# Kernel tuning notes

Measured on AMD Instinct MI355X. Metric: run time of the kernel, lower is better.

## Reference

```python
import jax, jax.numpy as jnp
import numpy as np

B, S, D = 2, 2048, 2048
H, KVH, HD = 32, 8, 64
ROPE_THETA = 500000.0


def _rope_cos_sin(seq_len, head_dim, theta, batch):
    inv_freq = 1.0 / (theta ** (jnp.arange(0, head_dim, 2, dtype=jnp.float32) / head_dim))  # [HD/2]
    pos = jnp.arange(seq_len, dtype=jnp.float32)
    freqs = jnp.outer(pos, inv_freq)                      # [S, HD/2]
    emb = jnp.concatenate([freqs, freqs], axis=-1)        # [S, HD]
    cos = jnp.broadcast_to(jnp.cos(emb), (batch, seq_len, head_dim))
    sin = jnp.broadcast_to(jnp.sin(emb), (batch, seq_len, head_dim))
    return cos, sin


def setup_inputs() -> dict:
    key = jax.random.key(0)
    kx, kq, kk, kv, ko = jax.random.split(key, 5)
    x = jax.random.normal(kx, (B, S, D), dtype=jnp.float32)
    cos, sin = _rope_cos_sin(S, HD, ROPE_THETA, B)
    scale = 0.02
    Wq = jax.random.normal(kq, (H * HD, D), dtype=jnp.float32) * scale
    Wk = jax.random.normal(kk, (KVH * HD, D), dtype=jnp.float32) * scale
    Wv = jax.random.normal(kv, (KVH * HD, D), dtype=jnp.float32) * scale
    Wo = jax.random.normal(ko, (D, H * HD), dtype=jnp.float32) * scale
    return {"x": x, "cos": cos, "sin": sin, "Wq": Wq, "Wk": Wk, "Wv": Wv, "Wo": Wo}


def rotate_half(t):
    t1, t2 = jnp.split(t, 2, axis=-1)
    return jnp.concatenate([-t2, t1], axis=-1)


def reference(x, cos, sin, Wq, Wk, Wv, Wo):
    b, s, d = x.shape
    scaling = HD ** -0.5
    groups = H // KVH
    # projections (torch Linear: y = x @ W.T)
    q = jnp.einsum('bsd,od->bso', x, Wq).reshape(b, s, H, HD).transpose(0, 2, 1, 3)    # [B,H,S,HD]
    k = jnp.einsum('bsd,od->bso', x, Wk).reshape(b, s, KVH, HD).transpose(0, 2, 1, 3)  # [B,KVH,S,HD]
    v = jnp.einsum('bsd,od->bso', x, Wv).reshape(b, s, KVH, HD).transpose(0, 2, 1, 3)
    # RoPE (cos/sin unsqueezed over head dim)
    c = cos[:, None, :, :]
    sn = sin[:, None, :, :]
    q = q * c + rotate_half(q) * sn
    k = k * c + rotate_half(k) * sn
    # GQA: repeat kv heads
    k = jnp.repeat(k, groups, axis=1)  # [B,H,S,HD]
    v = jnp.repeat(v, groups, axis=1)
    # causal eager SDPA
    scores = jnp.einsum('bhqd,bhkd->bhqk', q, k) * scaling
    causal = jnp.tril(jnp.ones((s, s), dtype=bool))
    scores = jnp.where(causal[None, None], scores, jnp.finfo(scores.dtype).min)
    attn_weights = jax.nn.softmax(scores, axis=-1)
    attn = jnp.einsum('bhqk,bhkd->bhqd', attn_weights, v)
    attn = attn.transpose(0, 2, 1, 3).reshape(b, s, H * HD)
    out = jnp.einsum('bso,do->bsd', attn, Wo)
    return out
```

## Files before the change

### kernel.cpp

```cpp
#include <hip/hip_runtime.h>
#include <hip/hip_bf16.h>

typedef __attribute__((ext_vector_type(8))) short bf16x8_t;
typedef __attribute__((ext_vector_type(4))) float f32x4;

#define S_LEN  2048
#define NB     2
#define NH     32
#define NKVH   8
#define HD     64
#define DMODEL 2048
#define SCALE  0.125f

__device__ __forceinline__ void gload16(const __hip_bfloat16* g, __hip_bfloat16* l) {
  __builtin_amdgcn_global_load_lds(
      (const __attribute__((address_space(1))) void*)g,
      (__attribute__((address_space(3))) void*)l, 16, 0, 0);
}

struct CvtSeg { const float* src; __hip_bfloat16* dst; int n4; };
struct CvtArgs { CvtSeg s[5]; };

__global__ __launch_bounds__(256) void cvt_all(CvtArgs a) {
  int i = blockIdx.x * blockDim.x + threadIdx.x;
#pragma unroll
  for (int k = 0; k < 5; ++k) {
    if (i < a.s[k].n4) {
      float4 v = ((const float4*)a.s[k].src)[i];
      __hip_bfloat16 o0 = __float2bfloat16(v.x), o1 = __float2bfloat16(v.y);
      __hip_bfloat16 o2 = __float2bfloat16(v.z), o3 = __float2bfloat16(v.w);
      ushort4 pk;
      pk.x = *(unsigned short*)&o0; pk.y = *(unsigned short*)&o1;
      pk.z = *(unsigned short*)&o2; pk.w = *(unsigned short*)&o3;
      ((ushort4*)a.s[k].dst)[i] = pk;
      return;
    }
    i -= a.s[k].n4;
  }
}

__global__ __launch_bounds__(256)
void gemm_qkv(const __hip_bfloat16* __restrict__ A,
              const __hip_bfloat16* __restrict__ Wq,
              const __hip_bfloat16* __restrict__ Wk,
              const __hip_bfloat16* __restrict__ Wv,
              __hip_bfloat16* __restrict__ Qo,
              __hip_bfloat16* __restrict__ Ko,
              __hip_bfloat16* __restrict__ Vto,
              const float* __restrict__ cosb,
              const float* __restrict__ sinb)
{
  __shared__ __align__(16) __hip_bfloat16 As[2][128][32];
  __shared__ __align__(16) __hip_bfloat16 Bs[2][128][32];
  const int K = DMODEL;

  const int tid  = threadIdx.x;
  const int lane = tid & 63;
  const int w    = tid >> 6;
  const int wr   = (w >> 1) * 64;
  const int wc   = (w & 1) * 64;
  const int brow = blockIdx.y * 128;
  const int fr   = lane & 15;
  const int fg   = lane >> 4;

  const int bc = blockIdx.x * 128;
  const __hip_bfloat16* Bt; int bcol; int path;
  if (bc < 2048)      { Bt = Wq; bcol = bc;        path = 0; }
  else if (bc < 2560) { Bt = Wk; bcol = bc - 2048; path = 1; }
  else                { Bt = Wv; bcol = bc - 2560; path = 2; }

  const f32x4 fz = {0.f, 0.f, 0.f, 0.f};
  f32x4 acc[4][4];
#pragma unroll
  for (int i = 0; i < 4; ++i)
#pragma unroll
    for (int j = 0; j < 4; ++j) acc[i][j] = fz;

  const int lrow = lane >> 2;
  const int lcol = (lane & 3) * 8;
  const __hip_bfloat16* Ag = A  + (size_t)(brow + w * 32 + lrow) * K + lcol;
  const __hip_bfloat16* Bg = Bt + (size_t)(bcol + w * 32 + lrow) * K + lcol;

  auto stage = [&](int buf, int kt) {
    gload16(Ag + kt,                    &As[buf][w * 32][0]);
    gload16(Ag + (size_t)16 * K + kt,   &As[buf][w * 32 + 16][0]);
    gload16(Bg + kt,                    &Bs[buf][w * 32][0]);
    gload16(Bg + (size_t)16 * K + kt,   &Bs[buf][w * 32 + 16][0]);
  };

  stage(0, 0);
  __syncthreads();
  int cur = 0;
  for (int kt = 0; kt < K; kt += 32) {
    if (kt + 32 < K) stage(cur ^ 1, kt + 32);

    bf16x8_t af[4], bfr[4];
#pragma unroll
    for (int mi = 0; mi < 4; ++mi)
      af[mi] = *(const bf16x8_t*)&As[cur][wr + mi * 16 + fr][fg * 8];
#pragma unroll
    for (int ni = 0; ni < 4; ++ni)
      bfr[ni] = *(const bf16x8_t*)&Bs[cur][wc + ni * 16 + fr][fg * 8];
#pragma unroll
    for (int mi = 0; mi < 4; ++mi)
#pragma unroll
      for (int ni = 0; ni < 4; ++ni)
        acc[mi][ni] = __builtin_amdgcn_mfma_f32_16x16x32_bf16(af[mi], bfr[ni], acc[mi][ni], 0, 0, 0);

    __syncthreads();
    cur ^= 1;
  }

  if (path == 2) {
#pragma unroll
    for (int mi = 0; mi < 4; ++mi) {
#pragma unroll
      for (int ni = 0; ni < 4; ++ni) {
        const int row0 = brow + wr + mi * 16 + fg * 4;
        const int col  = bcol + wc + ni * 16 + fr;
        const int b = row0 >> 11, s = row0 & 2047;
        const int kvh = col >> 6, d = col & 63;
        __hip_bfloat16 v0 = __float2bfloat16(acc[mi][ni][0]);
        __hip_bfloat16 v1 = __float2bfloat16(acc[mi][ni][1]);
        __hip_bfloat16 v2 = __float2bfloat16(acc[mi][ni][2]);
        __hip_bfloat16 v3 = __float2bfloat16(acc[mi][ni][3]);
        ushort4 pk;
        pk.x = *(unsigned short*)&v0; pk.y = *(unsigned short*)&v1;
        pk.z = *(unsigned short*)&v2; pk.w = *(unsigned short*)&v3;
        *(ushort4*)&Vto[(((size_t)b * NKVH + kvh) * HD + d) * S_LEN + s] = pk;
      }
    }
  } else {
    __hip_bfloat16* C = (path == 0) ? Qo : Ko;
    const int N = (path == 0) ? (NH * HD) : (NKVH * HD);
#pragma unroll
    for (int mi = 0; mi < 4; ++mi) {
#pragma unroll
      for (int r = 0; r < 4; ++r) {
        const int row = brow + wr + mi * 16 + fg * 4 + r;
#pragma unroll
        for (int ni = 0; ni < 2; ++ni) {
          const int colL = bcol + wc + ni * 16 + fr;
          const int d    = (colL & 63);
          const float c  = cosb[(size_t)row * HD + d];
          const float sn = sinb[(size_t)row * HD + d];
          const float v0 = acc[mi][ni][r];
          const float v1 = acc[mi][ni + 2][r];
          C[(size_t)row * N + colL]      = __float2bfloat16(v0 * c - v1 * sn);
          C[(size_t)row * N + colL + 32] = __float2bfloat16(v1 * c + v0 * sn);
        }
      }
    }
  }
}

__global__ __launch_bounds__(256)
void gemm_o(const __hip_bfloat16* __restrict__ A,
            const __hip_bfloat16* __restrict__ Bt,
            float* __restrict__ C)
{
  __shared__ __align__(16) __hip_bfloat16 As[2][128][32];
  __shared__ __align__(16) __hip_bfloat16 Bs[2][128][32];
  const int K = DMODEL, N = DMODEL;

  const int tid  = threadIdx.x;
  const int lane = tid & 63;
  const int w    = tid >> 6;
  const int wr   = (w >> 1) * 64;
  const int wc   = (w & 1) * 64;
  const int brow = blockIdx.y * 128;
  const int bcol = blockIdx.x * 128;
  const int fr   = lane & 15;
  const int fg   = lane >> 4;

  const f32x4 fz = {0.f, 0.f, 0.f, 0.f};
  f32x4 acc[4][4];
#pragma unroll
  for (int i = 0; i < 4; ++i)
#pragma unroll
    for (int j = 0; j < 4; ++j) acc[i][j] = fz;

  const int lrow = lane >> 2;
  const int lcol = (lane & 3) * 8;
  const __hip_bfloat16* Ag = A  + (size_t)(brow + w * 32 + lrow) * K + lcol;
  const __hip_bfloat16* Bg = Bt + (size_t)(bcol + w * 32 + lrow) * K + lcol;

  auto stage = [&](int buf, int kt) {
    gload16(Ag + kt,                  &As[buf][w * 32][0]);
    gload16(Ag + (size_t)16 * K + kt, &As[buf][w * 32 + 16][0]);
    gload16(Bg + kt,                  &Bs[buf][w * 32][0]);
    gload16(Bg + (size_t)16 * K + kt, &Bs[buf][w * 32 + 16][0]);
  };

  stage(0, 0);
  __syncthreads();
  int cur = 0;
  for (int kt = 0; kt < K; kt += 32) {
    if (kt + 32 < K) stage(cur ^ 1, kt + 32);

    bf16x8_t af[4], bfr[4];
#pragma unroll
    for (int mi = 0; mi < 4; ++mi)
      af[mi] = *(const bf16x8_t*)&As[cur][wr + mi * 16 + fr][fg * 8];
#pragma unroll
    for (int ni = 0; ni < 4; ++ni)
      bfr[ni] = *(const bf16x8_t*)&Bs[cur][wc + ni * 16 + fr][fg * 8];
#pragma unroll
    for (int mi = 0; mi < 4; ++mi)
#pragma unroll
      for (int ni = 0; ni < 4; ++ni)
        acc[mi][ni] = __builtin_amdgcn_mfma_f32_16x16x32_bf16(af[mi], bfr[ni], acc[mi][ni], 0, 0, 0);

    __syncthreads();
    cur ^= 1;
  }

#pragma unroll
  for (int mi = 0; mi < 4; ++mi)
#pragma unroll
    for (int ni = 0; ni < 4; ++ni) {
      const int row0 = brow + wr + mi * 16 + fg * 4;
      const int col  = bcol + wc + ni * 16 + fr;
#pragma unroll
      for (int r = 0; r < 4; ++r)
        C[(size_t)(row0 + r) * N + col] = acc[mi][ni][r];
    }
}

__global__ __launch_bounds__(256)
void attn_kernel(const __hip_bfloat16* __restrict__ Q, const __hip_bfloat16* __restrict__ K,
                 const __hip_bfloat16* __restrict__ Vt, __hip_bfloat16* __restrict__ O)
{
  __shared__ __align__(16) __hip_bfloat16 Ks[2][64][64];
  __shared__ __align__(16) __hip_bfloat16 Vs[2][64][64];
  __shared__ __align__(16) __hip_bfloat16 Ps[4][2][16][72];

  const int lane = threadIdx.x & 63;
  const int w    = threadIdx.x >> 6;
  const int fr   = lane & 15;
  const int fg   = lane >> 4;
  const int r8   = lane >> 3;
  const int j8   = lane & 7;
  const int bh   = blockIdx.y;
  const int b    = bh >> 5;
  const int h    = bh & 31;
  const int kvh  = h >> 2;
  const int qt    = gridDim.x - 1 - blockIdx.x;
  const int qbase = qt * 128;

  const __hip_bfloat16* Qg = Q + ((size_t)(b * S_LEN + qbase)) * DMODEL + h * HD;
  const __hip_bfloat16* Kg = K + (size_t)b * S_LEN * (NKVH * HD) + kvh * HD;
  const __hip_bfloat16* Vg = Vt + ((size_t)(b * NKVH + kvh)) * HD * S_LEN;

  bf16x8_t qf[2][2];
#pragma unroll
  for (int s = 0; s < 2; ++s)
#pragma unroll
    for (int kk = 0; kk < 2; ++kk)
      qf[s][kk] = *(const bf16x8_t*)(Qg + (size_t)(w * 32 + s * 16 + fr) * DMODEL + kk * 32 + fg * 8);

  const f32x4 fz = {0.f, 0.f, 0.f, 0.f};
  f32x4 acc[2][4];
#pragma unroll
  for (int s = 0; s < 2; ++s)
#pragma unroll
    for (int i = 0; i < 4; ++i) acc[s][i] = fz;
  float m_[2] = {-1e30f, -1e30f}, l_[2] = {0.f, 0.f};

  auto stage = [&](int buf, int kt) {
#pragma unroll
    for (int half = 0; half < 2; ++half) {
      const int row = w * 16 + half * 8 + r8;
      gload16(Kg + (size_t)(kt + row) * (NKVH * HD) + (j8 ^ r8) * 8, &Ks[buf][w * 16 + half * 8][0]);
      gload16(Vg + (size_t)row * S_LEN + kt + (j8 ^ r8) * 8,         &Vs[buf][w * 16 + half * 8][0]);
    }
  };
  auto ldK = [&](int buf, int row, int cidx) -> bf16x8_t {
    return *(const bf16x8_t*)&Ks[buf][row][(cidx ^ (row & 7)) * 8];
  };
  auto ldV = [&](int buf, int row, int cidx) -> bf16x8_t {
    return *(const bf16x8_t*)&Vs[buf][row][(cidx ^ (row & 7)) * 8];
  };

  stage(0, 0);
  __syncthreads();
  int cur = 0;
  const int NT = 2 * qt + 2;
  for (int t = 0; t < NT; ++t) {
    const int kt = t * 64;
    if (t + 1 < NT) stage(cur ^ 1, kt + 64);

    f32x4 sc[2][4];
#pragma unroll
    for (int c = 0; c < 4; ++c) {
      const int krow = c * 16 + fr;
      bf16x8_t k0 = ldK(cur, krow, fg);
      bf16x8_t k1 = ldK(cur, krow, 4 + fg);
      sc[0][c] = __builtin_amdgcn_mfma_f32_16x16x32_bf16(k0, qf[0][0], fz, 0, 0, 0);
      sc[0][c] = __builtin_amdgcn_mfma_f32_16x16x32_bf16(k1, qf[0][1], sc[0][c], 0, 0, 0);
      sc[1][c] = __builtin_amdgcn_mfma_f32_16x16x32_bf16(k0, qf[1][0], fz, 0, 0, 0);
      sc[1][c] = __builtin_amdgcn_mfma_f32_16x16x32_bf16(k1, qf[1][1], sc[1][c], 0, 0, 0);
    }

#pragma unroll
    for (int s = 0; s < 2; ++s) {
      const int base_s = qbase + w * 32 + s * 16;
      float p[4][4];
      float tm = -1e30f;
      if (kt + 63 > base_s) {
#pragma unroll
        for (int c = 0; c < 4; ++c)
#pragma unroll
          for (int r = 0; r < 4; ++r) {
            float v = sc[s][c][r] * SCALE;
            if (kt + c * 16 + fg * 4 + r > base_s + fr) v = -1e30f;
            p[c][r] = v; tm = fmaxf(tm, v);
          }
      } else {
#pragma unroll
        for (int c = 0; c < 4; ++c)
#pragma unroll
          for (int r = 0; r < 4; ++r) {
            float v = sc[s][c][r] * SCALE;
            p[c][r] = v; tm = fmaxf(tm, v);
          }
      }
      tm = fmaxf(tm, __shfl_xor(tm, 16));
      tm = fmaxf(tm, __shfl_xor(tm, 32));

      const float mnew = fmaxf(m_[s], tm);
      const float sf = __expf(m_[s] - mnew);
      m_[s] = mnew;

      float ts = 0.f;
#pragma unroll
      for (int c = 0; c < 4; ++c)
#pragma unroll
        for (int r = 0; r < 4; ++r) { p[c][r] = __expf(p[c][r] - mnew); ts += p[c][r]; }
      ts += __shfl_xor(ts, 16);
      ts += __shfl_xor(ts, 32);
      l_[s] = l_[s] * sf + ts;

      float sfv[4];
#pragma unroll
      for (int r = 0; r < 4; ++r) sfv[r] = __shfl(sf, fg * 4 + r);
#pragma unroll
      for (int fc = 0; fc < 4; ++fc)
#pragma unroll
        for (int r = 0; r < 4; ++r) acc[s][fc][r] *= sfv[r];

#pragma unroll
      for (int c = 0; c < 4; ++c) {
        __hip_bfloat16 b0 = __float2bfloat16(p[c][0]);
        __hip_bfloat16 b1 = __float2bfloat16(p[c][1]);
        __hip_bfloat16 b2 = __float2bfloat16(p[c][2]);
        __hip_bfloat16 b3 = __float2bfloat16(p[c][3]);
        ushort4 pk;
        pk.x = *(unsigned short*)&b0; pk.y = *(unsigned short*)&b1;
        pk.z = *(unsigned short*)&b2; pk.w = *(unsigned short*)&b3;
        *(ushort4*)&Ps[w][s][fr][c * 16 + fg * 4] = pk;
      }
    }

#pragma unroll
    for (int kk = 0; kk < 2; ++kk) {
      bf16x8_t pa0 = *(const bf16x8_t*)&Ps[w][0][fr][kk * 32 + fg * 8];
      bf16x8_t pa1 = *(const bf16x8_t*)&Ps[w][1][fr][kk * 32 + fg * 8];
#pragma unroll
      for (int fc = 0; fc < 4; ++fc) {
        bf16x8_t vf = ldV(cur, fc * 16 + fr, kk * 4 + fg);
        acc[0][fc] = __builtin_amdgcn_mfma_f32_16x16x32_bf16(pa0, vf, acc[0][fc], 0, 0, 0);
        acc[1][fc] = __builtin_amdgcn_mfma_f32_16x16x32_bf16(pa1, vf, acc[1][fc], 0, 0, 0);
      }
    }

    __syncthreads();
    cur ^= 1;
  }

  float lv[2][4];
#pragma unroll
  for (int s = 0; s < 2; ++s)
#pragma unroll
    for (int r = 0; r < 4; ++r)
      lv[s][r] = __builtin_amdgcn_rcpf(__shfl(l_[s], fg * 4 + r));
#pragma unroll
  for (int s = 0; s < 2; ++s)
#pragma unroll
    for (int fc = 0; fc < 4; ++fc)
#pragma unroll
      for (int r = 0; r < 4; ++r) {
        const size_t row = (size_t)(b * S_LEN + qbase + w * 32 + s * 16 + fg * 4 + r);
        O[row * DMODEL + h * HD + fc * 16 + fr] = __float2bfloat16(acc[s][fc][r] * lv[s][r]);
      }
}

extern "C" void kernel_launch(void* const* d_in, const int* in_sizes, int n_in,
                              void* d_out, int out_size, void* d_ws, size_t ws_size,
                              hipStream_t stream)
{
  const float* x    = (const float*)d_in[0];
  const float* cosb = (const float*)d_in[1];
  const float* sinb = (const float*)d_in[2];
  const float* Wq   = (const float*)d_in[3];
  const float* Wk   = (const float*)d_in[4];
  const float* Wv   = (const float*)d_in[5];
  const float* Wo   = (const float*)d_in[6];
  float* out = (float*)d_out;

  char* p = (char*)d_ws;
  __hip_bfloat16* x_bf    = (__hip_bfloat16*)p; p += (size_t)NB * S_LEN * DMODEL * 2;
  __hip_bfloat16* Wq_bf   = (__hip_bfloat16*)p; p += (size_t)NH * HD * DMODEL * 2;
  __hip_bfloat16* Wk_bf   = (__hip_bfloat16*)p; p += (size_t)NKVH * HD * DMODEL * 2;
  __hip_bfloat16* Wv_bf   = (__hip_bfloat16*)p; p += (size_t)NKVH * HD * DMODEL * 2;
  __hip_bfloat16* Wo_bf   = (__hip_bfloat16*)p; p += (size_t)DMODEL * NH * HD * 2;
  __hip_bfloat16* Q_bf    = (__hip_bfloat16*)p; p += (size_t)NB * S_LEN * NH * HD * 2;
  __hip_bfloat16* K_bf    = (__hip_bfloat16*)p; p += (size_t)NB * S_LEN * NKVH * HD * 2;
  __hip_bfloat16* Vt_bf   = (__hip_bfloat16*)p; p += (size_t)NB * NKVH * HD * S_LEN * 2;
  __hip_bfloat16* attn_bf = (__hip_bfloat16*)p; p += (size_t)NB * S_LEN * NH * HD * 2;

  CvtArgs ca;
  ca.s[0] = { x,  x_bf,  (int)((size_t)NB * S_LEN * DMODEL / 4) };
  ca.s[1] = { Wq, Wq_bf, (int)((size_t)NH * HD * DMODEL / 4) };
  ca.s[2] = { Wk, Wk_bf, (int)((size_t)NKVH * HD * DMODEL / 4) };
  ca.s[3] = { Wv, Wv_bf, (int)((size_t)NKVH * HD * DMODEL / 4) };
  ca.s[4] = { Wo, Wo_bf, (int)((size_t)DMODEL * NH * HD / 4) };
  int total4 = ca.s[0].n4 + ca.s[1].n4 + ca.s[2].n4 + ca.s[3].n4 + ca.s[4].n4;
  cvt_all<<<(total4 + 255) / 256, 256, 0, stream>>>(ca);

  const dim3 blk(256);
  gemm_qkv<<<dim3(3072 / 128, (NB * S_LEN) / 128), blk, 0, stream>>>(
      x_bf, Wq_bf, Wk_bf, Wv_bf, Q_bf, K_bf, Vt_bf, cosb, sinb);

  attn_kernel<<<dim3(S_LEN / 128, NB * NH), blk, 0, stream>>>(Q_bf, K_bf, Vt_bf, attn_bf);

  gemm_o<<<dim3(DMODEL / 128, (NB * S_LEN) / 128), blk, 0, stream>>>(attn_bf, Wo_bf, out);
}
```

Before: 410.9 us.

## Use 8 waves per attention block with lazy rescale and exp2 softmax

The attention kernel now runs 512 threads per block, each wave owning 16 query rows instead of 32. K and V staging is split between the two halves of the block. Waves skip tiles that lie fully above the causal diagonal, and the running max is rescaled only when the new max exceeds the old one by a threshold. Exponentials use exp2 with the softmax scale folded into one constant, and the row-sum reduction across lanes is deferred to the end. This aims to raise occupancy, remove wasted masked work and cut per-tile rescale cost, at the price of per-wave divergence around barriers and the numerical risk of the lazy-rescale threshold.

```diff
diff --git a/kernel.cpp b/kernel.cpp
--- a/kernel.cpp
+++ b/kernel.cpp
@@ -11,6 +11,8 @@
 #define HD     64
 #define DMODEL 2048
 #define SCALE  0.125f
+#define CEXP   0.18033688f
+#define THRRAW 44.0f
 
 __device__ __forceinline__ void gload16(const __hip_bfloat16* g, __hip_bfloat16* l) {
   __builtin_amdgcn_global_load_lds(
@@ -227,13 +229,13 @@
     }
 }
 
-__global__ __launch_bounds__(256)
+__global__ __launch_bounds__(512, 6)
 void attn_kernel(const __hip_bfloat16* __restrict__ Q, const __hip_bfloat16* __restrict__ K,
                  const __hip_bfloat16* __restrict__ Vt, __hip_bfloat16* __restrict__ O)
 {
   __shared__ __align__(16) __hip_bfloat16 Ks[2][64][64];
   __shared__ __align__(16) __hip_bfloat16 Vs[2][64][64];
-  __shared__ __align__(16) __hip_bfloat16 Ps[4][2][16][72];
+  __shared__ __align__(16) __hip_bfloat16 Ps[8][16][72];
 
   const int lane = threadIdx.x & 63;
   const int w    = threadIdx.x >> 6;
@@ -247,32 +249,32 @@
   const int kvh  = h >> 2;
   const int qt    = gridDim.x - 1 - blockIdx.x;
   const int qbase = qt * 128;
+  const int base_s = qbase + w * 16;
 
   const __hip_bfloat16* Qg = Q + ((size_t)(b * S_LEN + qbase)) * DMODEL + h * HD;
   const __hip_bfloat16* Kg = K + (size_t)b * S_LEN * (NKVH * HD) + kvh * HD;
   const __hip_bfloat16* Vg = Vt + ((size_t)(b * NKVH + kvh)) * HD * S_LEN;
 
-  bf16x8_t qf[2][2];
-#pragma unroll
-  for (int s = 0; s < 2; ++s)
-#pragma unroll
-    for (int kk = 0; kk < 2; ++kk)
-      qf[s][kk] = *(const bf16x8_t*)(Qg + (size_t)(w * 32 + s * 16 + fr) * DMODEL + kk * 32 + fg * 8);
+  bf16x8_t qf[2];
+#pragma unroll
+  for (int kk = 0; kk < 2; ++kk)
+    qf[kk] = *(const bf16x8_t*)(Qg + (size_t)(w * 16 + fr) * DMODEL + kk * 32 + fg * 8);
 
   const f32x4 fz = {0.f, 0.f, 0.f, 0.f};
-  f32x4 acc[2][4];
-#pragma unroll
-  for (int s = 0; s < 2; ++s)
-#pragma unroll
-    for (int i = 0; i < 4; ++i) acc[s][i] = fz;
-  float m_[2] = {-1e30f, -1e30f}, l_[2] = {0.f, 0.f};
+  f32x4 acc[4];
+#pragma unroll
+  for (int i = 0; i < 4; ++i) acc[i] = fz;
+  float m_ = -1e30f;
+  float l_ = 0.f;
 
   auto stage = [&](int buf, int kt) {
-#pragma unroll
-    for (int half = 0; half < 2; ++half) {
-      const int row = w * 16 + half * 8 + r8;
-      gload16(Kg + (size_t)(kt + row) * (NKVH * HD) + (j8 ^ r8) * 8, &Ks[buf][w * 16 + half * 8][0]);
-      gload16(Vg + (size_t)row * S_LEN + kt + (j8 ^ r8) * 8,         &Vs[buf][w * 16 + half * 8][0]);
+    const int rb = (w & 3) * 16;
+    if (w < 4) {
+      gload16(Kg + (size_t)(kt + rb + r8)     * (NKVH * HD) + (j8 ^ r8) * 8, &Ks[buf][rb][0]);
+      gload16(Kg + (size_t)(kt + rb + 8 + r8) * (NKVH * HD) + (j8 ^ r8) * 8, &Ks[buf][rb + 8][0]);
+    } else {
+      gload16(Vg + (size_t)(rb + r8)     * S_LEN + kt + (j8 ^ r8) * 8, &Vs[buf][rb][0]);
+      gload16(Vg + (size_t)(rb + 8 + r8) * S_LEN + kt + (j8 ^ r8) * 8, &Vs[buf][rb + 8][0]);
     }
   };
   auto ldK = [&](int buf, int row, int cidx) -> bf16x8_t {
@@ -290,64 +292,60 @@
     const int kt = t * 64;
     if (t + 1 < NT) stage(cur ^ 1, kt + 64);
 
-    f32x4 sc[2][4];
-#pragma unroll
-    for (int c = 0; c < 4; ++c) {
-      const int krow = c * 16 + fr;
-      bf16x8_t k0 = ldK(cur, krow, fg);
-      bf16x8_t k1 = ldK(cur, krow, 4 + fg);
-      sc[0][c] = __builtin_amdgcn_mfma_f32_16x16x32_bf16(k0, qf[0][0], fz, 0, 0, 0);
-      sc[0][c] = __builtin_amdgcn_mfma_f32_16x16x32_bf16(k1, qf[0][1], sc[0][c], 0, 0, 0);
-      sc[1][c] = __builtin_amdgcn_mfma_f32_16x16x32_bf16(k0, qf[1][0], fz, 0, 0, 0);
-      sc[1][c] = __builtin_amdgcn_mfma_f32_16x16x32_bf16(k1, qf[1][1], sc[1][c], 0, 0, 0);
-    }
-
-#pragma unroll
-    for (int s = 0; s < 2; ++s) {
-      const int base_s = qbase + w * 32 + s * 16;
+    if (kt <= base_s + 15) {
+      f32x4 sc[4];
+#pragma unroll
+      for (int c = 0; c < 4; ++c) {
+        const int krow = c * 16 + fr;
+        bf16x8_t k0 = ldK(cur, krow, fg);
+        bf16x8_t k1 = ldK(cur, krow, 4 + fg);
+        sc[c] = __builtin_amdgcn_mfma_f32_16x16x32_bf16(k0, qf[0], fz, 0, 0, 0);
+        sc[c] = __builtin_amdgcn_mfma_f32_16x16x32_bf16(k1, qf[1], sc[c], 0, 0, 0);
+      }
+
       float p[4][4];
-      float tm = -1e30f;
+      float tm = -3.0e38f;
       if (kt + 63 > base_s) {
 #pragma unroll
         for (int c = 0; c < 4; ++c)
 #pragma unroll
           for (int r = 0; r < 4; ++r) {
-            float v = sc[s][c][r] * SCALE;
-            if (kt + c * 16 + fg * 4 + r > base_s + fr) v = -1e30f;
+            float v = sc[c][r];
+            if (kt + c * 16 + fg * 4 + r > base_s + fr) v = -3.0e38f;
             p[c][r] = v; tm = fmaxf(tm, v);
           }
       } else {
 #pragma unroll
         for (int c = 0; c < 4; ++c)
 #pragma unroll
-          for (int r = 0; r < 4; ++r) {
-            float v = sc[s][c][r] * SCALE;
-            p[c][r] = v; tm = fmaxf(tm, v);
-          }
+          for (int r = 0; r < 4; ++r) { p[c][r] = sc[c][r]; tm = fmaxf(tm, sc[c][r]); }
       }
       tm = fmaxf(tm, __shfl_xor(tm, 16));
       tm = fmaxf(tm, __shfl_xor(tm, 32));
 
-      const float mnew = fmaxf(m_[s], tm);
-      const float sf = __expf(m_[s] - mnew);
-      m_[s] = mnew;
+      if (!__all(tm <= m_ + THRRAW)) {
+        const float mnew = fmaxf(m_, tm);
+        const float sf = exp2f((m_ - mnew) * CEXP);
+        m_ = mnew;
+        l_ *= sf;
+        float sfv[4];
+#pragma unroll
+        for (int r = 0; r < 4; ++r) sfv[r] = __shfl(sf, fg * 4 + r);
+#pragma unroll
+        for (int fc = 0; fc < 4; ++fc)
+#pragma unroll
+          for (int r = 0; r < 4; ++r) acc[fc][r] *= sfv[r];
+      }
 
       float ts = 0.f;
 #pragma unroll
       for (int c = 0; c < 4; ++c)
 #pragma unroll
-        for (int r = 0; r < 4; ++r) { p[c][r] = __expf(p[c][r] - mnew); ts += p[c][r]; }
-      ts += __shfl_xor(ts, 16);
-      ts += __shfl_xor(ts, 32);
-      l_[s] = l_[s] * sf + ts;
-
-      float sfv[4];
-#pragma unroll
-      for (int r = 0; r < 4; ++r) sfv[r] = __shfl(sf, fg * 4 + r);
-#pragma unroll
-      for (int fc = 0; fc < 4; ++fc)
-#pragma unroll
-        for (int r = 0; r < 4; ++r) acc[s][fc][r] *= sfv[r];
+        for (int r = 0; r < 4; ++r) {
+          p[c][r] = exp2f((p[c][r] - m_) * CEXP);
+          ts += p[c][r];
+        }
+      l_ += ts;
 
 #pragma unroll
       for (int c = 0; c < 4; ++c) {
@@ -358,19 +356,17 @@
         ushort4 pk;
         pk.x = *(unsigned short*)&b0; pk.y = *(unsigned short*)&b1;
         pk.z = *(unsigned short*)&b2; pk.w = *(unsigned short*)&b3;
-        *(ushort4*)&Ps[w][s][fr][c * 16 + fg * 4] = pk;
-      }
-    }
-
-#pragma unroll
-    for (int kk = 0; kk < 2; ++kk) {
-      bf16x8_t pa0 = *(const bf16x8_t*)&Ps[w][0][fr][kk * 32 + fg * 8];
-      bf16x8_t pa1 = *(const bf16x8_t*)&Ps[w][1][fr][kk * 32 + fg * 8];
-#pragma unroll
-      for (int fc = 0; fc < 4; ++fc) {
-        bf16x8_t vf = ldV(cur, fc * 16 + fr, kk * 4 + fg);
-        acc[0][fc] = __builtin_amdgcn_mfma_f32_16x16x32_bf16(pa0, vf, acc[0][fc], 0, 0, 0);
-        acc[1][fc] = __builtin_amdgcn_mfma_f32_16x16x32_bf16(pa1, vf, acc[1][fc], 0, 0, 0);
+        *(ushort4*)&Ps[w][fr][c * 16 + fg * 4] = pk;
+      }
+
+#pragma unroll
+      for (int kk = 0; kk < 2; ++kk) {
+        bf16x8_t pa = *(const bf16x8_t*)&Ps[w][fr][kk * 32 + fg * 8];
+#pragma unroll
+        for (int fc = 0; fc < 4; ++fc) {
+          bf16x8_t vf = ldV(cur, fc * 16 + fr, kk * 4 + fg);
+          acc[fc] = __builtin_amdgcn_mfma_f32_16x16x32_bf16(pa, vf, acc[fc], 0, 0, 0);
+        }
       }
     }
 
@@ -378,21 +374,18 @@
     cur ^= 1;
   }
 
-  float lv[2][4];
-#pragma unroll
-  for (int s = 0; s < 2; ++s)
-#pragma unroll
-    for (int r = 0; r < 4; ++r)
-      lv[s][r] = __builtin_amdgcn_rcpf(__shfl(l_[s], fg * 4 + r));
-#pragma unroll
-  for (int s = 0; s < 2; ++s)
-#pragma unroll
-    for (int fc = 0; fc < 4; ++fc)
-#pragma unroll
-      for (int r = 0; r < 4; ++r) {
-        const size_t row = (size_t)(b * S_LEN + qbase + w * 32 + s * 16 + fg * 4 + r);
-        O[row * DMODEL + h * HD + fc * 16 + fr] = __float2bfloat16(acc[s][fc][r] * lv[s][r]);
-      }
+  l_ += __shfl_xor(l_, 16);
+  l_ += __shfl_xor(l_, 32);
+  float lv[4];
+#pragma unroll
+  for (int r = 0; r < 4; ++r) lv[r] = __builtin_amdgcn_rcpf(__shfl(l_, fg * 4 + r));
+#pragma unroll
+  for (int fc = 0; fc < 4; ++fc)
+#pragma unroll
+    for (int r = 0; r < 4; ++r) {
+      const size_t row = (size_t)(b * S_LEN + base_s + fg * 4 + r);
+      O[row * DMODEL + h * HD + fc * 16 + fr] = __float2bfloat16(acc[fc][r] * lv[r]);
+    }
 }
 
 extern "C" void kernel_launch(void* const* d_in, const int* in_sizes, int n_in,
@@ -428,11 +421,10 @@
   int total4 = ca.s[0].n4 + ca.s[1].n4 + ca.s[2].n4 + ca.s[3].n4 + ca.s[4].n4;
   cvt_all<<<(total4 + 255) / 256, 256, 0, stream>>>(ca);
 
-  const dim3 blk(256);
-  gemm_qkv<<<dim3(3072 / 128, (NB * S_LEN) / 128), blk, 0, stream>>>(
+  gemm_qkv<<<dim3(3072 / 128, (NB * S_LEN) / 128), dim3(256), 0, stream>>>(
       x_bf, Wq_bf, Wk_bf, Wv_bf, Q_bf, K_bf, Vt_bf, cosb, sinb);
 
-  attn_kernel<<<dim3(S_LEN / 128, NB * NH), blk, 0, stream>>>(Q_bf, K_bf, Vt_bf, attn_bf);
-
-  gemm_o<<<dim3(DMODEL / 128, (NB * S_LEN) / 128), blk, 0, stream>>>(attn_bf, Wo_bf, out);
-}
+  attn_kernel<<<dim3(S_LEN / 128, NB * NH), dim3(512), 0, stream>>>(Q_bf, K_bf, Vt_bf, attn_bf);
+
+  gemm_o<<<dim3(DMODEL / 128, (NB * S_LEN) / 128), dim3(256), 0, stream>>>(attn_bf, Wo_bf, out);
+}
```

Result: faster. 377.3 us (-8.2%).
